# Performance work log

Hardware: AMD Instinct MI355X
Metric: run time of the kernel (lower is better)

Reference implementation:

```python
import jax, jax.numpy as jnp
import numpy as np

WS = 4          # cubic window size
NUM_HEADS = 4
CF = 64         # fused_channels
DIM = 2 * CF    # attention dim (concat of two projected streams)


def _rel_pos_index(w):
    coords = np.stack(np.meshgrid(np.arange(w), np.arange(w), np.arange(w), indexing='ij'))
    cf = coords.reshape(3, -1)                      # [3, N]
    rel = cf[:, :, None] - cf[:, None, :]           # [3, N, N]
    rel = rel.transpose(1, 2, 0) + (w - 1)          # shift to >= 0
    idx = rel[..., 0] * (2 * w - 1) ** 2 + rel[..., 1] * (2 * w - 1) + rel[..., 2]
    return idx.astype(np.int32)                     # [N, N]


def _window_partition(x, w):
    # x: [B, D, H, W, C] -> [B*nW, w^3, C]
    B, D, H, W, C = x.shape
    x = x.reshape(B, D // w, w, H // w, w, W // w, w, C)
    x = x.transpose(0, 1, 3, 5, 2, 4, 6, 7)
    return x.reshape(-1, w * w * w, C)


def _window_reverse(x, w, B, D, H, W):
    C = x.shape[-1]
    x = x.reshape(B, D // w, H // w, W // w, w, w, w, C)
    x = x.transpose(0, 1, 4, 2, 5, 3, 6, 7)
    return x.reshape(B, D, H, W, C)


def setup_inputs() -> dict:
    key = jax.random.key(0)
    ks = jax.random.split(key, 12)
    B, Cc, Ct, S = 1, 64, 64, 64
    inp = {
        'conv_feat': jax.random.normal(ks[0], (B, Cc, S, S, S), jnp.float32),
        'transformer_feat': jax.random.normal(ks[1], (B, Ct, S, S, S), jnp.float32),
        # 1x1x1 conv projections -> plain channel matmuls
        'conv_w': jax.random.normal(ks[2], (CF, Cc), jnp.float32) * 0.05,
        'conv_b': jnp.zeros((CF,), jnp.float32),
        'trans_w': jax.random.normal(ks[3], (CF, Ct), jnp.float32) * 0.05,
        'trans_b': jnp.zeros((CF,), jnp.float32),
        # window attention params (dim = 2*CF)
        'qkv_w': jax.random.normal(ks[4], (3 * DIM, DIM), jnp.float32) * 0.05,
        'qkv_b': jnp.zeros((3 * DIM,), jnp.float32),
        'proj_w': jax.random.normal(ks[5], (DIM, DIM), jnp.float32) * 0.05,
        'proj_b': jnp.zeros((DIM,), jnp.float32),
        'rel_bias_table': jax.random.normal(ks[6], ((2 * WS - 1) ** 3, NUM_HEADS), jnp.float32) * 0.02,
        'rel_index': jnp.asarray(_rel_pos_index(WS)),
    }
    return inp


def reference(conv_feat, transformer_feat, conv_w, conv_b, trans_w, trans_b,
              qkv_w, qkv_b, proj_w, proj_b, rel_bias_table, rel_index):
    B, Cc, D, H, W = conv_feat.shape
    # 1x1x1 conv projections
    cp = jnp.einsum('bcdhw,oc->bodhw', conv_feat, conv_w) + conv_b[None, :, None, None, None]
    tp = jnp.einsum('bcdhw,oc->bodhw', transformer_feat, trans_w) + trans_b[None, :, None, None, None]
    combined = jnp.concatenate([cp, tp], axis=1)            # [B, 2CF, D, H, W]

    # windowed self-attention (Swin-3D style, relative position bias)
    x = jnp.transpose(combined, (0, 2, 3, 4, 1))            # [B, D, H, W, 2CF]
    xw = _window_partition(x, WS)                           # [nB, N, DIM], N = WS^3
    nB, N, _ = xw.shape
    hd = DIM // NUM_HEADS
    qkv = xw @ qkv_w.T + qkv_b                              # [nB, N, 3*DIM]
    qkv = qkv.reshape(nB, N, 3, NUM_HEADS, hd).transpose(2, 0, 3, 1, 4)
    q, k, v = qkv[0], qkv[1], qkv[2]                        # [nB, h, N, hd]
    attn = jnp.einsum('bhnd,bhmd->bhnm', q * (hd ** -0.5), k)
    bias = rel_bias_table[rel_index.reshape(-1)].reshape(N, N, NUM_HEADS)
    attn = attn + jnp.transpose(bias, (2, 0, 1))[None]      # [nB, h, N, N]
    attn = jax.nn.softmax(attn, axis=-1)
    out = jnp.einsum('bhnm,bhmd->bhnd', attn, v)            # [nB, h, N, hd]
    out = out.transpose(0, 2, 1, 3).reshape(nB, N, DIM)
    out = out @ proj_w.T + proj_b

    x = _window_reverse(out, WS, B, D, H, W)                # [B, D, H, W, DIM]
    fused = jnp.transpose(x, (0, 4, 1, 2, 3))               # [B, DIM, D, H, W]

    conv_fused = fused[:, :CF]
    trans_fused = fused[:, CF:]
    return conv_fused + trans_fused + conv_feat
```

## Files before the change

### kernel.cpp

```cpp
#include <hip/hip_runtime.h>


typedef __attribute__((ext_vector_type(8))) short bf16x8;
typedef __attribute__((ext_vector_type(4))) float f32x4;

__device__ __forceinline__ unsigned short f2b(float f) {
    union { float f; unsigned int i; } v; v.f = f;
    unsigned int i = v.i;
    return (unsigned short)((i + 0x7FFFu + ((i >> 16) & 1u)) >> 16);
}

#define WSB_BYTE_OFF 147456

__global__ __launch_bounds__(256) void prep_kernel(
    const float* __restrict__ conv_w, const float* __restrict__ trans_w,
    const float* __restrict__ qkv_w, const float* __restrict__ proj_w,
    const float* __restrict__ btab, const int* __restrict__ ridx,
    unsigned short* __restrict__ wsW, float* __restrict__ wsB)
{
    int id = blockIdx.x * 256 + threadIdx.x;
    if (id < 9216) {
        int lane = id & 63;
        int colr = lane & 15, quad = lane >> 4;
        const float* src;
        float scale = 1.0f;
        if (id < 512) {
            int tile = id >> 6; int rt = tile >> 1, kt = tile & 1;
            src = conv_w + (rt * 16 + colr) * 64 + kt * 32 + quad * 8;
        } else if (id < 1024) {
            int tile = (id - 512) >> 6; int rt = tile >> 1, kt = tile & 1;
            src = trans_w + (rt * 16 + colr) * 64 + kt * 32 + quad * 8;
        } else if (id < 7168) {
            int tile = (id - 1024) >> 6; int rt = tile >> 2, kt = tile & 3;
            int r = rt * 16 + colr;
            src = qkv_w + r * 128 + kt * 32 + quad * 8;
            if (r < 128) scale = 0.17677669529663689f;
        } else {
            int tile = (id - 7168) >> 6; int rt = tile >> 2, kt = tile & 3;
            src = proj_w + (rt * 16 + colr) * 128 + kt * 32 + quad * 8;
        }
        bf16x8 r;
#pragma unroll
        for (int j = 0; j < 8; ++j) r[j] = (short)f2b(src[j] * scale);
        *reinterpret_cast<bf16x8*>(wsW + id * 8) = r;
    } else if (id < 13312) {
        int i = id - 9216;
        int h = i >> 10, nt = (i >> 8) & 3, mt = (i >> 6) & 3, lane = i & 63;
        int colr = lane & 15, quad = lane >> 4;
        f32x4 o;
#pragma unroll
        for (int g = 0; g < 4; ++g) {
            int n = nt * 16 + quad * 4 + g, m = mt * 16 + colr;
            o[g] = btab[ridx[n * 64 + m] * 4 + h];
        }
        *reinterpret_cast<f32x4*>(wsB + i * 4) = o;
    }
}

#define REG_A 0
#define REG_B 8192
#define REG_C 16384

__device__ __forceinline__ int idx128(int base, int t, int c) {
    int swz = ((c >> 3) ^ (t & 15) ^ ((t >> 4) & 3)) & 15;
    return base + t * 128 + (swz << 3) + (c & 7);
}
__device__ __forceinline__ int idxqk(int base, int h, int t, int d) {
    int swz = ((d >> 3) ^ (t & 3) ^ ((t >> 2) & 3)) & 3;
    return base + h * 2048 + t * 32 + (swz << 3) + (d & 7);
}
__device__ __forceinline__ int idxv(int h, int d, int m) {
    int swz = ((m >> 3) ^ (d & 7)) & 7;
    return REG_C + h * 2048 + d * 64 + (swz << 3) + (m & 7);
}
__device__ __forceinline__ int idxp(int h, int n, int m) {
    int swz = ((m >> 3) ^ (n & 7)) & 7;
    return h * 4096 + n * 64 + (swz << 3) + (m & 7);
}
__device__ __forceinline__ int idxfu(int c, int t) {
    int swz = ((t >> 2) ^ (c & 15)) & 15;
    return c * 64 + (swz << 2) + (t & 3);
}

__global__ __launch_bounds__(256, 3) void win_attn_kernel(
    const float* __restrict__ cfeat,
    const float* __restrict__ tfeat,
    const float* __restrict__ conv_b,
    const float* __restrict__ trans_b,
    const float* __restrict__ qkv_b,
    const float* __restrict__ proj_b,
    const unsigned short* __restrict__ wsW,
    const float* __restrict__ wsB,
    float* __restrict__ out)
{
    __shared__ unsigned short smem[24576];
    float* fuf = reinterpret_cast<float*>(&smem[REG_B]);

    const int tid  = threadIdx.x;
    const int lane = tid & 63;
    const int wv   = tid >> 6;
    const int col  = lane & 15;
    const int quad = lane >> 4;

    int b   = blockIdx.x;
    int wid = ((b & 7) << 9) | (b >> 3);
    int wz = wid >> 8, wy = (wid >> 4) & 15, wx = wid & 15;
    const int vbase = wz * 16384 + wy * 256 + wx * 4;

#pragma unroll
    for (int it = 0; it < 4; ++it) {
        int id = tid + (it << 8);
        int cg = id >> 6;
        int t  = id & 63;
        int inp = cg >> 3;
        int c0  = (cg & 7) << 3;
        const float* src = (inp ? tfeat : cfeat) + (size_t)c0 * 262144 + vbase
                         + ((t >> 4) << 12) + (((t >> 2) & 3) << 6) + (t & 3);
        bf16x8 r;
#pragma unroll
        for (int j = 0; j < 8; ++j) r[j] = (short)f2b(src[(size_t)j * 262144]);
        *reinterpret_cast<bf16x8*>(&smem[idx128(REG_A, t, inp * 64 + c0)]) = r;
    }
    __syncthreads();

    {
        int half = wv >> 1;
        const float* bvec = half ? trans_b : conv_b;
        bf16x8 afr[4][2];
#pragma unroll
        for (int tt = 0; tt < 4; ++tt)
#pragma unroll
            for (int kt = 0; kt < 2; ++kt)
                afr[tt][kt] = *reinterpret_cast<const bf16x8*>(
                    &smem[idx128(REG_A, tt * 16 + col, half * 64 + kt * 32 + quad * 8)]);
#pragma unroll
        for (int otl = 0; otl < 2; ++otl) {
            int rt  = (wv & 1) * 2 + otl;
            int row = rt * 16 + col;
            bf16x8 bfr[2];
#pragma unroll
            for (int kt = 0; kt < 2; ++kt)
                bfr[kt] = *reinterpret_cast<const bf16x8*>(
                    wsW + (half * 512 + (rt * 2 + kt) * 64 + lane) * 8);
            float bias = bvec[row];
            int oc = half * 64 + row;
#pragma unroll
            for (int tt = 0; tt < 4; ++tt) {
                f32x4 acc = {0.f, 0.f, 0.f, 0.f};
#pragma unroll
                for (int kt = 0; kt < 2; ++kt)
                    acc = __builtin_amdgcn_mfma_f32_16x16x32_bf16(afr[tt][kt], bfr[kt], acc, 0, 0, 0);
#pragma unroll
                for (int g = 0; g < 4; ++g)
                    smem[idx128(REG_B, tt * 16 + quad * 4 + g, oc)] = f2b(acc[g] + bias);
            }
        }
    }
    __syncthreads();

    {
        bf16x8 afr[4][4];
#pragma unroll
        for (int tt = 0; tt < 4; ++tt)
#pragma unroll
            for (int kt = 0; kt < 4; ++kt)
                afr[tt][kt] = *reinterpret_cast<const bf16x8*>(
                    &smem[idx128(REG_B, tt * 16 + col, kt * 32 + quad * 8)]);
        __syncthreads();
        for (int rt = wv * 6; rt < wv * 6 + 6; ++rt) {
            int r = rt * 16 + col;
            bf16x8 bfr[4];
#pragma unroll
            for (int kt = 0; kt < 4; ++kt)
                bfr[kt] = *reinterpret_cast<const bf16x8*>(
                    wsW + (1024 + (rt * 4 + kt) * 64 + lane) * 8);
            float bias = qkv_b[r];
            int sel = r >> 7;
            int h   = (r >> 5) & 3;
            int d0  = r & 31;
            if (sel == 0) bias *= 0.17677669529663689f;
#pragma unroll
            for (int tt = 0; tt < 4; ++tt) {
                f32x4 acc = {0.f, 0.f, 0.f, 0.f};
#pragma unroll
                for (int kt = 0; kt < 4; ++kt)
                    acc = __builtin_amdgcn_mfma_f32_16x16x32_bf16(afr[tt][kt], bfr[kt], acc, 0, 0, 0);
#pragma unroll
                for (int g = 0; g < 4; ++g) {
                    int t = tt * 16 + quad * 4 + g;
                    float v = acc[g] + bias;
                    if (sel == 0)      smem[idxqk(REG_A, h, t, d0)] = f2b(v);
                    else if (sel == 1) smem[idxqk(REG_B, h, t, d0)] = f2b(v);
                    else               smem[idxv(h, d0, t)] = f2b(v);
                }
            }
        }
    }
    __syncthreads();

    float inv[4][4];
    {
        const int h = wv;
        bf16x8 qfr[4], kfr[4];
#pragma unroll
        for (int nt = 0; nt < 4; ++nt) {
            qfr[nt] = *reinterpret_cast<const bf16x8*>(&smem[idxqk(REG_A, h, nt * 16 + col, quad * 8)]);
            kfr[nt] = *reinterpret_cast<const bf16x8*>(&smem[idxqk(REG_B, h, nt * 16 + col, quad * 8)]);
        }
        __syncthreads();
#pragma unroll
        for (int nt = 0; nt < 4; ++nt) {
            f32x4 s[4];
#pragma unroll
            for (int mt = 0; mt < 4; ++mt) {
                f32x4 binit = *reinterpret_cast<const f32x4*>(
                    wsB + ((h * 1024 + nt * 256 + mt * 64 + lane) << 2));
                s[mt] = __builtin_amdgcn_mfma_f32_16x16x32_bf16(qfr[nt], kfr[mt], binit, 0, 0, 0);
            }
#pragma unroll
            for (int g = 0; g < 4; ++g) {
                float e0 = __expf(fminf(s[0][g], 80.f));
                float e1 = __expf(fminf(s[1][g], 80.f));
                float e2 = __expf(fminf(s[2][g], 80.f));
                float e3 = __expf(fminf(s[3][g], 80.f));
                float sm = (e0 + e1) + (e2 + e3);
#pragma unroll
                for (int o = 1; o < 16; o <<= 1) sm += __shfl_xor(sm, o, 64);
                inv[nt][g] = 1.0f / sm;
                s[0][g] = e0; s[1][g] = e1; s[2][g] = e2; s[3][g] = e3;
            }
#pragma unroll
            for (int mt = 0; mt < 4; ++mt) {
                int m = mt * 16 + col;
#pragma unroll
                for (int g = 0; g < 4; ++g)
                    smem[idxp(h, nt * 16 + quad * 4 + g, m)] = f2b(s[mt][g]);
            }
        }
    }
    __syncthreads();

    {
        const int h = wv;
        bf16x8 pfr[4][2], vfr[2][2];
#pragma unroll
        for (int dt = 0; dt < 2; ++dt)
#pragma unroll
            for (int kt = 0; kt < 2; ++kt)
                vfr[dt][kt] = *reinterpret_cast<const bf16x8*>(
                    &smem[idxv(h, dt * 16 + col, kt * 32 + quad * 8)]);
#pragma unroll
        for (int nt = 0; nt < 4; ++nt)
#pragma unroll
            for (int kt = 0; kt < 2; ++kt)
                pfr[nt][kt] = *reinterpret_cast<const bf16x8*>(
                    &smem[idxp(h, nt * 16 + col, kt * 32 + quad * 8)]);
        __syncthreads();
#pragma unroll
        for (int nt = 0; nt < 4; ++nt)
#pragma unroll
            for (int dt = 0; dt < 2; ++dt) {
                f32x4 acc = {0.f, 0.f, 0.f, 0.f};
#pragma unroll
                for (int kt = 0; kt < 2; ++kt)
                    acc = __builtin_amdgcn_mfma_f32_16x16x32_bf16(pfr[nt][kt], vfr[dt][kt], acc, 0, 0, 0);
#pragma unroll
                for (int g = 0; g < 4; ++g)
                    smem[idx128(REG_A, nt * 16 + quad * 4 + g, h * 32 + dt * 16 + col)] =
                        f2b(acc[g] * inv[nt][g]);
            }
    }
    __syncthreads();

    {
        bf16x8 afr[4][4];
#pragma unroll
        for (int tt = 0; tt < 4; ++tt)
#pragma unroll
            for (int kt = 0; kt < 4; ++kt)
                afr[tt][kt] = *reinterpret_cast<const bf16x8*>(
                    &smem[idx128(REG_A, tt * 16 + col, kt * 32 + quad * 8)]);
        int o1 = wv * 16 + col;
        int o2 = 64 + o1;
        bf16x8 b1[4], b2[4];
#pragma unroll
        for (int kt = 0; kt < 4; ++kt) {
            b1[kt] = *reinterpret_cast<const bf16x8*>(wsW + (7168 + (wv * 4 + kt) * 64 + lane) * 8);
            b2[kt] = *reinterpret_cast<const bf16x8*>(wsW + (7168 + ((4 + wv) * 4 + kt) * 64 + lane) * 8);
        }
        float pb = proj_b[o1] + proj_b[o2];
#pragma unroll
        for (int tt = 0; tt < 4; ++tt) {
            f32x4 a1 = {0.f, 0.f, 0.f, 0.f}, a2 = {0.f, 0.f, 0.f, 0.f};
#pragma unroll
            for (int kt = 0; kt < 4; ++kt) {
                a1 = __builtin_amdgcn_mfma_f32_16x16x32_bf16(afr[tt][kt], b1[kt], a1, 0, 0, 0);
                a2 = __builtin_amdgcn_mfma_f32_16x16x32_bf16(afr[tt][kt], b2[kt], a2, 0, 0, 0);
            }
            f32x4 o;
#pragma unroll
            for (int g = 0; g < 4; ++g) o[g] = a1[g] + a2[g] + pb;
            *reinterpret_cast<f32x4*>(&fuf[idxfu(o1, tt * 16 + quad * 4)]) = o;
        }
    }
    __syncthreads();

#pragma unroll
    for (int it = 0; it < 4; ++it) {
        int id = tid + (it << 8);
        int c  = id >> 4;
        int z  = (id >> 2) & 3, y = id & 3;
        int t  = z * 16 + y * 4;
        f32x4 val = *reinterpret_cast<const f32x4*>(&fuf[idxfu(c, t)]);
        const float* rp = cfeat + (size_t)c * 262144 + vbase + z * 4096 + y * 64;
        f32x4 res = *reinterpret_cast<const f32x4*>(rp);
        f32x4 o;
#pragma unroll
        for (int g = 0; g < 4; ++g) o[g] = val[g] + res[g];
        *reinterpret_cast<f32x4*>(out + (size_t)c * 262144 + vbase + z * 4096 + y * 64) = o;
    }
}

extern "C" void kernel_launch(void* const* d_in, const int* in_sizes, int n_in,
                              void* d_out, int out_size, void* d_ws, size_t ws_size,
                              hipStream_t stream) {
    (void)in_sizes; (void)n_in; (void)out_size; (void)ws_size;
    unsigned short* wsW = (unsigned short*)d_ws;
    float* wsB = (float*)((char*)d_ws + WSB_BYTE_OFF);

    prep_kernel<<<dim3(52), dim3(256), 0, stream>>>(
        (const float*)d_in[2],
        (const float*)d_in[4],
        (const float*)d_in[6],
        (const float*)d_in[8],
        (const float*)d_in[10],
        (const int*)d_in[11],
        wsW, wsB);

    win_attn_kernel<<<dim3(4096), dim3(256), 0, stream>>>(
        (const float*)d_in[0],
        (const float*)d_in[1],
        (const float*)d_in[3],
        (const float*)d_in[5],
        (const float*)d_in[7],
        (const float*)d_in[9],
        wsW, wsB,
        (float*)d_out);
}
```

Baseline: 318.5 us.

## Fuse per-head QKV projection into attention using register fragments and bpermute

Each wave now computes its own head's Q, K and V directly from the shared fused features. MFMA outputs are reshaped into operand fragments with ds_bpermute instead of round-tripping Q/K/V and probabilities through LDS. This removes the QKV and P staging regions and several barriers, cutting LDS from 48KB to 32KB so occupancy can go from 3 to 4 blocks. In exchange it adds many bpermute ops, reloads the shared A fragments per tile, and computes S transposed, which requires a reordered bias table.

```diff
diff --git a/kernel.cpp b/kernel.cpp
--- a/kernel.cpp
+++ b/kernel.cpp
@@ -8,6 +8,32 @@
     union { float f; unsigned int i; } v; v.f = f;
     unsigned int i = v.i;
     return (unsigned short)((i + 0x7FFFu + ((i >> 16) & 1u)) >> 16);
+}
+__device__ __forceinline__ unsigned int pkman(float a, float b) {
+    return ((unsigned int)f2b(b) << 16) | (unsigned int)f2b(a);
+}
+
+union U8 { bf16x8 v; unsigned int u[4]; };
+
+__device__ __forceinline__ bf16x8 xfrag(const f32x4 lo, const f32x4 hi,
+                                        int aA, int aB, bool hiq) {
+    unsigned int l0 = pkman(lo[0], lo[1]), l1 = pkman(lo[2], lo[3]);
+    unsigned int h0 = pkman(hi[0], hi[1]), h1 = pkman(hi[2], hi[3]);
+    U8 r;
+    unsigned int tl, th;
+    tl = (unsigned int)__builtin_amdgcn_ds_bpermute(aA, (int)l0);
+    th = (unsigned int)__builtin_amdgcn_ds_bpermute(aA, (int)h0);
+    r.u[0] = hiq ? th : tl;
+    tl = (unsigned int)__builtin_amdgcn_ds_bpermute(aA, (int)l1);
+    th = (unsigned int)__builtin_amdgcn_ds_bpermute(aA, (int)h1);
+    r.u[1] = hiq ? th : tl;
+    tl = (unsigned int)__builtin_amdgcn_ds_bpermute(aB, (int)l0);
+    th = (unsigned int)__builtin_amdgcn_ds_bpermute(aB, (int)h0);
+    r.u[2] = hiq ? th : tl;
+    tl = (unsigned int)__builtin_amdgcn_ds_bpermute(aB, (int)l1);
+    th = (unsigned int)__builtin_amdgcn_ds_bpermute(aB, (int)h1);
+    r.u[3] = hiq ? th : tl;
+    return r.v;
 }
 
 #define WSB_BYTE_OFF 147456
@@ -45,12 +71,13 @@
         *reinterpret_cast<bf16x8*>(wsW + id * 8) = r;
     } else if (id < 13312) {
         int i = id - 9216;
-        int h = i >> 10, nt = (i >> 8) & 3, mt = (i >> 6) & 3, lane = i & 63;
+        int h = i >> 10, mt = (i >> 8) & 3, nt = (i >> 6) & 3, lane = i & 63;
         int colr = lane & 15, quad = lane >> 4;
         f32x4 o;
 #pragma unroll
         for (int g = 0; g < 4; ++g) {
-            int n = nt * 16 + quad * 4 + g, m = mt * 16 + colr;
+            int n = nt * 16 + colr;
+            int m = mt * 16 + quad * 4 + g;
             o[g] = btab[ridx[n * 64 + m] * 4 + h];
         }
         *reinterpret_cast<f32x4*>(wsB + i * 4) = o;
@@ -59,30 +86,17 @@
 
 #define REG_A 0
 #define REG_B 8192
-#define REG_C 16384
 
 __device__ __forceinline__ int idx128(int base, int t, int c) {
-    int swz = ((c >> 3) ^ (t & 15) ^ ((t >> 4) & 3)) & 15;
+    int swz = ((c >> 3) ^ (t & 15)) & 15;
     return base + t * 128 + (swz << 3) + (c & 7);
-}
-__device__ __forceinline__ int idxqk(int base, int h, int t, int d) {
-    int swz = ((d >> 3) ^ (t & 3) ^ ((t >> 2) & 3)) & 3;
-    return base + h * 2048 + t * 32 + (swz << 3) + (d & 7);
-}
-__device__ __forceinline__ int idxv(int h, int d, int m) {
-    int swz = ((m >> 3) ^ (d & 7)) & 7;
-    return REG_C + h * 2048 + d * 64 + (swz << 3) + (m & 7);
-}
-__device__ __forceinline__ int idxp(int h, int n, int m) {
-    int swz = ((m >> 3) ^ (n & 7)) & 7;
-    return h * 4096 + n * 64 + (swz << 3) + (m & 7);
 }
 __device__ __forceinline__ int idxfu(int c, int t) {
     int swz = ((t >> 2) ^ (c & 15)) & 15;
     return c * 64 + (swz << 2) + (t & 3);
 }
 
-__global__ __launch_bounds__(256, 3) void win_attn_kernel(
+__global__ __launch_bounds__(256, 4) void win_attn_kernel(
     const float* __restrict__ cfeat,
     const float* __restrict__ tfeat,
     const float* __restrict__ conv_b,
@@ -93,7 +107,7 @@
     const float* __restrict__ wsB,
     float* __restrict__ out)
 {
-    __shared__ unsigned short smem[24576];
+    __shared__ unsigned short smem[16384];
     float* fuf = reinterpret_cast<float*>(&smem[REG_B]);
 
     const int tid  = threadIdx.x;
@@ -116,10 +130,13 @@
         int c0  = (cg & 7) << 3;
         const float* src = (inp ? tfeat : cfeat) + (size_t)c0 * 262144 + vbase
                          + ((t >> 4) << 12) + (((t >> 2) & 3) << 6) + (t & 3);
-        bf16x8 r;
-#pragma unroll
-        for (int j = 0; j < 8; ++j) r[j] = (short)f2b(src[(size_t)j * 262144]);
-        *reinterpret_cast<bf16x8*>(&smem[idx128(REG_A, t, inp * 64 + c0)]) = r;
+        float f[8];
+#pragma unroll
+        for (int j = 0; j < 8; ++j) f[j] = src[(size_t)j * 262144];
+        U8 r;
+#pragma unroll
+        for (int j = 0; j < 4; ++j) r.u[j] = pkman(f[2 * j], f[2 * j + 1]);
+        *reinterpret_cast<bf16x8*>(&smem[idx128(REG_A, t, inp * 64 + c0)]) = r.v;
     }
     __syncthreads();
 
@@ -150,125 +167,157 @@
 #pragma unroll
                 for (int kt = 0; kt < 2; ++kt)
                     acc = __builtin_amdgcn_mfma_f32_16x16x32_bf16(afr[tt][kt], bfr[kt], acc, 0, 0, 0);
-#pragma unroll
-                for (int g = 0; g < 4; ++g)
-                    smem[idx128(REG_B, tt * 16 + quad * 4 + g, oc)] = f2b(acc[g] + bias);
+                unsigned int pA = pkman(acc[0] + bias, acc[1] + bias);
+                unsigned int pB = pkman(acc[2] + bias, acc[3] + bias);
+                int t0 = tt * 16 + quad * 4;
+                smem[idx128(REG_B, t0 + 0, oc)] = (unsigned short)(pA & 0xffff);
+                smem[idx128(REG_B, t0 + 1, oc)] = (unsigned short)(pA >> 16);
+                smem[idx128(REG_B, t0 + 2, oc)] = (unsigned short)(pB & 0xffff);
+                smem[idx128(REG_B, t0 + 3, oc)] = (unsigned short)(pB >> 16);
             }
         }
     }
     __syncthreads();
 
-    {
-        bf16x8 afr[4][4];
-#pragma unroll
-        for (int tt = 0; tt < 4; ++tt)
-#pragma unroll
-            for (int kt = 0; kt < 4; ++kt)
-                afr[tt][kt] = *reinterpret_cast<const bf16x8*>(
-                    &smem[idx128(REG_B, tt * 16 + col, kt * 32 + quad * 8)]);
-        __syncthreads();
-        for (int rt = wv * 6; rt < wv * 6 + 6; ++rt) {
-            int r = rt * 16 + col;
-            bf16x8 bfr[4];
-#pragma unroll
-            for (int kt = 0; kt < 4; ++kt)
-                bfr[kt] = *reinterpret_cast<const bf16x8*>(
-                    wsW + (1024 + (rt * 4 + kt) * 64 + lane) * 8);
-            float bias = qkv_b[r];
-            int sel = r >> 7;
-            int h   = (r >> 5) & 3;
-            int d0  = r & 31;
-            if (sel == 0) bias *= 0.17677669529663689f;
-#pragma unroll
-            for (int tt = 0; tt < 4; ++tt) {
-                f32x4 acc = {0.f, 0.f, 0.f, 0.f};
-#pragma unroll
-                for (int kt = 0; kt < 4; ++kt)
-                    acc = __builtin_amdgcn_mfma_f32_16x16x32_bf16(afr[tt][kt], bfr[kt], acc, 0, 0, 0);
-#pragma unroll
-                for (int g = 0; g < 4; ++g) {
-                    int t = tt * 16 + quad * 4 + g;
-                    float v = acc[g] + bias;
-                    if (sel == 0)      smem[idxqk(REG_A, h, t, d0)] = f2b(v);
-                    else if (sel == 1) smem[idxqk(REG_B, h, t, d0)] = f2b(v);
-                    else               smem[idxv(h, d0, t)] = f2b(v);
-                }
-            }
-        }
-    }
-    __syncthreads();
-
-    float inv[4][4];
     {
         const int h = wv;
-        bf16x8 qfr[4], kfr[4];
+        const int aA = ((((2 * quad) & 3) << 4) | col) << 2;
+        const int aB = ((((2 * quad + 1) & 3) << 4) | col) << 2;
+        const bool hiq = quad >= 2;
+
+        float4 qb4[2], kb4[2]; float vb2[2];
+#pragma unroll
+        for (int dt = 0; dt < 2; ++dt) {
+            float4 q = *reinterpret_cast<const float4*>(qkv_b + h * 32 + dt * 16 + quad * 4);
+            q.x *= 0.17677669529663689f; q.y *= 0.17677669529663689f;
+            q.z *= 0.17677669529663689f; q.w *= 0.17677669529663689f;
+            qb4[dt] = q;
+            kb4[dt] = *reinterpret_cast<const float4*>(qkv_b + 128 + h * 32 + dt * 16 + quad * 4);
+            vb2[dt] = qkv_b[256 + h * 32 + dt * 16 + col];
+        }
+
+        bf16x8 qb[4], kb[4], vfr[2][2];
+
+#pragma unroll
+        for (int dt = 0; dt < 2; ++dt) {
+            bf16x8 w[4];
+#pragma unroll
+            for (int kt = 0; kt < 4; ++kt)
+                w[kt] = *reinterpret_cast<const bf16x8*>(
+                    wsW + (1024 + ((16 + 2 * h + dt) * 4 + kt) * 64 + lane) * 8);
+            f32x4 vt[4];
+#pragma unroll
+            for (int tt = 0; tt < 4; ++tt) {
+                bf16x8 a[4];
+#pragma unroll
+                for (int kt = 0; kt < 4; ++kt)
+                    a[kt] = *reinterpret_cast<const bf16x8*>(
+                        &smem[idx128(REG_B, tt * 16 + col, kt * 32 + quad * 8)]);
+                f32x4 acc = {0.f, 0.f, 0.f, 0.f};
+#pragma unroll
+                for (int kt = 0; kt < 4; ++kt)
+                    acc = __builtin_amdgcn_mfma_f32_16x16x32_bf16(a[kt], w[kt], acc, 0, 0, 0);
+#pragma unroll
+                for (int g = 0; g < 4; ++g) acc[g] += vb2[dt];
+                vt[tt] = acc;
+            }
+            vfr[dt][0] = xfrag(vt[0], vt[1], aA, aB, hiq);
+            vfr[dt][1] = xfrag(vt[2], vt[3], aA, aB, hiq);
+        }
+
 #pragma unroll
         for (int nt = 0; nt < 4; ++nt) {
-            qfr[nt] = *reinterpret_cast<const bf16x8*>(&smem[idxqk(REG_A, h, nt * 16 + col, quad * 8)]);
-            kfr[nt] = *reinterpret_cast<const bf16x8*>(&smem[idxqk(REG_B, h, nt * 16 + col, quad * 8)]);
-        }
-        __syncthreads();
+            bf16x8 a[4];
+#pragma unroll
+            for (int kt = 0; kt < 4; ++kt)
+                a[kt] = *reinterpret_cast<const bf16x8*>(
+                    &smem[idx128(REG_B, nt * 16 + col, kt * 32 + quad * 8)]);
+            f32x4 qa[2];
+#pragma unroll
+            for (int dt = 0; dt < 2; ++dt) {
+                bf16x8 w[4];
+#pragma unroll
+                for (int kt = 0; kt < 4; ++kt)
+                    w[kt] = *reinterpret_cast<const bf16x8*>(
+                        wsW + (1024 + ((2 * h + dt) * 4 + kt) * 64 + lane) * 8);
+                f32x4 acc = {0.f, 0.f, 0.f, 0.f};
+#pragma unroll
+                for (int kt = 0; kt < 4; ++kt)
+                    acc = __builtin_amdgcn_mfma_f32_16x16x32_bf16(w[kt], a[kt], acc, 0, 0, 0);
+                acc[0] += qb4[dt].x; acc[1] += qb4[dt].y;
+                acc[2] += qb4[dt].z; acc[3] += qb4[dt].w;
+                qa[dt] = acc;
+            }
+            qb[nt] = xfrag(qa[0], qa[1], aA, aB, hiq);
+        }
+
+#pragma unroll
+        for (int mt = 0; mt < 4; ++mt) {
+            bf16x8 a[4];
+#pragma unroll
+            for (int kt = 0; kt < 4; ++kt)
+                a[kt] = *reinterpret_cast<const bf16x8*>(
+                    &smem[idx128(REG_B, mt * 16 + col, kt * 32 + quad * 8)]);
+            f32x4 ka[2];
+#pragma unroll
+            for (int dt = 0; dt < 2; ++dt) {
+                bf16x8 w[4];
+#pragma unroll
+                for (int kt = 0; kt < 4; ++kt)
+                    w[kt] = *reinterpret_cast<const bf16x8*>(
+                        wsW + (1024 + ((8 + 2 * h + dt) * 4 + kt) * 64 + lane) * 8);
+                f32x4 acc = {0.f, 0.f, 0.f, 0.f};
+#pragma unroll
+                for (int kt = 0; kt < 4; ++kt)
+                    acc = __builtin_amdgcn_mfma_f32_16x16x32_bf16(w[kt], a[kt], acc, 0, 0, 0);
+                acc[0] += kb4[dt].x; acc[1] += kb4[dt].y;
+                acc[2] += kb4[dt].z; acc[3] += kb4[dt].w;
+                ka[dt] = acc;
+            }
+            kb[mt] = xfrag(ka[0], ka[1], aA, aB, hiq);
+        }
+
 #pragma unroll
         for (int nt = 0; nt < 4; ++nt) {
-            f32x4 s[4];
+            f32x4 st[4];
 #pragma unroll
             for (int mt = 0; mt < 4; ++mt) {
                 f32x4 binit = *reinterpret_cast<const f32x4*>(
-                    wsB + ((h * 1024 + nt * 256 + mt * 64 + lane) << 2));
-                s[mt] = __builtin_amdgcn_mfma_f32_16x16x32_bf16(qfr[nt], kfr[mt], binit, 0, 0, 0);
-            }
-#pragma unroll
-            for (int g = 0; g < 4; ++g) {
-                float e0 = __expf(fminf(s[0][g], 80.f));
-                float e1 = __expf(fminf(s[1][g], 80.f));
-                float e2 = __expf(fminf(s[2][g], 80.f));
-                float e3 = __expf(fminf(s[3][g], 80.f));
-                float sm = (e0 + e1) + (e2 + e3);
-#pragma unroll
-                for (int o = 1; o < 16; o <<= 1) sm += __shfl_xor(sm, o, 64);
-                inv[nt][g] = 1.0f / sm;
-                s[0][g] = e0; s[1][g] = e1; s[2][g] = e2; s[3][g] = e3;
-            }
-#pragma unroll
-            for (int mt = 0; mt < 4; ++mt) {
-                int m = mt * 16 + col;
-#pragma unroll
-                for (int g = 0; g < 4; ++g)
-                    smem[idxp(h, nt * 16 + quad * 4 + g, m)] = f2b(s[mt][g]);
-            }
-        }
-    }
-    __syncthreads();
-
-    {
-        const int h = wv;
-        bf16x8 pfr[4][2], vfr[2][2];
-#pragma unroll
-        for (int dt = 0; dt < 2; ++dt)
-#pragma unroll
-            for (int kt = 0; kt < 2; ++kt)
-                vfr[dt][kt] = *reinterpret_cast<const bf16x8*>(
-                    &smem[idxv(h, dt * 16 + col, kt * 32 + quad * 8)]);
-#pragma unroll
-        for (int nt = 0; nt < 4; ++nt)
-#pragma unroll
-            for (int kt = 0; kt < 2; ++kt)
-                pfr[nt][kt] = *reinterpret_cast<const bf16x8*>(
-                    &smem[idxp(h, nt * 16 + col, kt * 32 + quad * 8)]);
-        __syncthreads();
-#pragma unroll
-        for (int nt = 0; nt < 4; ++nt)
+                    wsB + ((((h * 4 + mt) * 4 + nt) * 64 + lane) << 2));
+                st[mt] = __builtin_amdgcn_mfma_f32_16x16x32_bf16(kb[mt], qb[nt], binit, 0, 0, 0);
+            }
+            float sm = 0.f;
+#pragma unroll
+            for (int mt = 0; mt < 4; ++mt)
+#pragma unroll
+                for (int g = 0; g < 4; ++g) {
+                    st[mt][g] = __expf(fminf(st[mt][g], 80.f));
+                    sm += st[mt][g];
+                }
+            sm += __shfl_xor(sm, 16, 64);
+            sm += __shfl_xor(sm, 32, 64);
+            float inv = 1.0f / sm;
+#pragma unroll
+            for (int mt = 0; mt < 4; ++mt)
+#pragma unroll
+                for (int g = 0; g < 4; ++g) st[mt][g] *= inv;
+            bf16x8 pa0 = xfrag(st[0], st[1], aA, aB, hiq);
+            bf16x8 pa1 = xfrag(st[2], st[3], aA, aB, hiq);
 #pragma unroll
             for (int dt = 0; dt < 2; ++dt) {
-                f32x4 acc = {0.f, 0.f, 0.f, 0.f};
-#pragma unroll
-                for (int kt = 0; kt < 2; ++kt)
-                    acc = __builtin_amdgcn_mfma_f32_16x16x32_bf16(pfr[nt][kt], vfr[dt][kt], acc, 0, 0, 0);
-#pragma unroll
-                for (int g = 0; g < 4; ++g)
-                    smem[idx128(REG_A, nt * 16 + quad * 4 + g, h * 32 + dt * 16 + col)] =
-                        f2b(acc[g] * inv[nt][g]);
-            }
+                f32x4 o = {0.f, 0.f, 0.f, 0.f};
+                o = __builtin_amdgcn_mfma_f32_16x16x32_bf16(pa0, vfr[dt][0], o, 0, 0, 0);
+                o = __builtin_amdgcn_mfma_f32_16x16x32_bf16(pa1, vfr[dt][1], o, 0, 0, 0);
+                int c  = h * 32 + dt * 16 + col;
+                int t0 = nt * 16 + quad * 4;
+                unsigned int pA = pkman(o[0], o[1]);
+                unsigned int pB = pkman(o[2], o[3]);
+                smem[idx128(REG_A, t0 + 0, c)] = (unsigned short)(pA & 0xffff);
+                smem[idx128(REG_A, t0 + 1, c)] = (unsigned short)(pA >> 16);
+                smem[idx128(REG_A, t0 + 2, c)] = (unsigned short)(pB & 0xffff);
+                smem[idx128(REG_A, t0 + 3, c)] = (unsigned short)(pB >> 16);
+            }
+        }
     }
     __syncthreads();
 
@@ -312,8 +361,7 @@
         int z  = (id >> 2) & 3, y = id & 3;
         int t  = z * 16 + y * 4;
         f32x4 val = *reinterpret_cast<const f32x4*>(&fuf[idxfu(c, t)]);
-        const float* rp = cfeat + (size_t)c * 262144 + vbase + z * 4096 + y * 64;
-        f32x4 res = *reinterpret_cast<const f32x4*>(rp);
+        f32x4 res = *reinterpret_cast<const f32x4*>(cfeat + (size_t)c * 262144 + vbase + z * 4096 + y * 64);
         f32x4 o;
 #pragma unroll
         for (int g = 0; g < 4; ++g) o[g] = val[g] + res[g];
```

Result: slower. 490.6 us (+54.1%).
